# Kernel tuning notes

Measured on AMD Instinct MI355X. Metric: run time of the kernel, lower is better.

## Reference

```python
import jax, jax.numpy as jnp
import numpy as np

B, C, H, W = 4, 256, 64, 64
D = C // 8  # qk projection dim = 32


def setup_inputs() -> dict:
    key = jax.random.key(0)
    ks = jax.random.split(key, 10)
    s = 1.0 / np.sqrt(C)
    return {
        "semantic_map": jax.random.normal(ks[0], (B, C, H, W), jnp.float32),
        "structural_map": jax.random.normal(ks[1], (B, C, H, W), jnp.float32),
        "Wq": jax.random.normal(ks[2], (D, C), jnp.float32) * s,
        "bq": jax.random.normal(ks[3], (D,), jnp.float32) * 0.01,
        "Wk": jax.random.normal(ks[4], (D, C), jnp.float32) * s,
        "bk": jax.random.normal(ks[5], (D,), jnp.float32) * 0.01,
        "Wv": jax.random.normal(ks[6], (C, C), jnp.float32) * s,
        "bv": jax.random.normal(ks[7], (C,), jnp.float32) * 0.01,
        "gamma": jnp.zeros((1,), jnp.float32) + 0.5,  # nonzero so the attention path matters
    }


def reference(semantic_map, structural_map, Wq, bq, Wk, bk, Wv, bv, gamma):
    b, c, h, w = semantic_map.shape
    n = h * w
    # 1x1 convs == per-pixel linear projections
    q = jnp.einsum("bchw,dc->bdhw", semantic_map, Wq) + bq[None, :, None, None]
    k = jnp.einsum("bchw,dc->bdhw", structural_map, Wk) + bk[None, :, None, None]
    v = jnp.einsum("bchw,oc->bohw", structural_map, Wv) + bv[None, :, None, None]
    q = q.reshape(b, -1, n).transpose(0, 2, 1)  # (B, HW, D)
    k = k.reshape(b, -1, n)                     # (B, D, HW)
    v = v.reshape(b, c, n)                      # (B, C, HW)
    energy = jnp.einsum("bid,bdj->bij", q, k)   # (B, HW, HW)
    attention = jax.nn.softmax(energy, axis=-1)
    # out[b,c,i] = sum_j v[b,c,j] * attention[b,i,j]
    out = jnp.einsum("bcj,bij->bci", v, attention).reshape(b, c, h, w)
    return gamma * out + semantic_map
```

## Files before the change

### kernel.cpp

```cpp
#include <hip/hip_runtime.h>

#define B_   4
#define C_   256
#define N_   4096
#define D_   32
#define CP   264

typedef _Float16 half8  __attribute__((ext_vector_type(8)));
typedef _Float16 half4v __attribute__((ext_vector_type(4)));
typedef _Float16 half2v __attribute__((ext_vector_type(2)));
typedef float    f32x4  __attribute__((ext_vector_type(4)));

__global__ __launch_bounds__(256) void wcvt_kernel(
    const float* __restrict__ Wq, const float* __restrict__ Wk,
    const float* __restrict__ Wv, _Float16* __restrict__ Wh)
{
    const int idx = blockIdx.x * 256 + threadIdx.x;
    const int kk  = idx & 31;
    const int row = (idx >> 5) & 15;
    const int kc  = (idx >> 9) & 7;
    const int t   = idx >> 12;
    const int c   = kc*32 + kk;
    float v;
    if (t < 2)      v = Wq[(t*16 + row)*C_ + c];
    else if (t < 4) v = Wk[((t-2)*16 + row)*C_ + c];
    else            v = Wv[((t-4)*16 + row)*C_ + c];
    Wh[idx] = (_Float16)v;
}

__global__ __launch_bounds__(256, 2) void proj_kernel(
    const float* __restrict__ sem, const float* __restrict__ str,
    const _Float16* __restrict__ Wh,
    const float* __restrict__ bq, const float* __restrict__ bk,
    const float* __restrict__ bv,
    _Float16* __restrict__ Qh, _Float16* __restrict__ Kh, _Float16* __restrict__ Vh2)
{
    __shared__ __align__(16) _Float16 s_x[64 * CP];
    __shared__ __align__(16) _Float16 s_s[64 * CP];

    const int bid = blockIdx.x;
    const int h   = bid & 1;
    const int nt6 = (bid >> 1) & 63;
    const int b   = bid >> 7;
    const int n0  = nt6 * 64;
    const int tid = threadIdx.x;
    const int w    = tid >> 6;
    const int lane = tid & 63;
    const int quad = lane >> 4;
    const int l15  = lane & 15;

    const int cnt = (w < 2) ? 3 : 2;
    const int t0  = h*10 + ((w < 2) ? w*3 : 6 + (w-2)*2);
    const bool need_sem = (h == 0);

    f32x4 acc[3][4];
    #pragma unroll
    for (int i = 0; i < 3; ++i)
        #pragma unroll
        for (int j = 0; j < 4; ++j) { acc[i][j][0]=0.f; acc[i][j][1]=0.f; acc[i][j][2]=0.f; acc[i][j][3]=0.f; }

    const size_t xbase = (size_t)b * C_ * N_;

    #pragma unroll
    for (int r = 0; r < 8; ++r) {
        const int slot = r*256 + tid;
        const int nq = slot & 15;
        const int cp = slot >> 4;
        const float* p0 = str + xbase + (size_t)(2*cp) * N_ + n0 + nq*4;
        const float4 a4 = *(const float4*)p0;
        const float4 b4 = *(const float4*)(p0 + N_);
        #pragma unroll
        for (int t = 0; t < 4; ++t) {
            half2v hp; hp[0] = (_Float16)a4[t]; hp[1] = (_Float16)b4[t];
            *(half2v*)(s_x + (nq*4 + t)*CP + 2*cp) = hp;
        }
        if (need_sem) {
            const float* p1 = sem + xbase + (size_t)(2*cp) * N_ + n0 + nq*4;
            const float4 c4 = *(const float4*)p1;
            const float4 d4 = *(const float4*)(p1 + N_);
            #pragma unroll
            for (int t = 0; t < 4; ++t) {
                half2v hp; hp[0] = (_Float16)c4[t]; hp[1] = (_Float16)d4[t];
                *(half2v*)(s_s + (nq*4 + t)*CP + 2*cp) = hp;
            }
        }
    }
    __syncthreads();

    #pragma unroll 1
    for (int kc = 0; kc < 8; ++kc) {
        half8 bfr[4], sfr[4];
        #pragma unroll
        for (int nt = 0; nt < 4; ++nt)
            bfr[nt] = *(const half8*)(s_x + (nt*16 + l15)*CP + kc*32 + quad*8);
        if (w == 0 && need_sem) {
            #pragma unroll
            for (int nt = 0; nt < 4; ++nt)
                sfr[nt] = *(const half8*)(s_s + (nt*16 + l15)*CP + kc*32 + quad*8);
        }
        #pragma unroll
        for (int mi = 0; mi < 3; ++mi) {
            if (mi >= cnt) break;
            const int t = t0 + mi;
            half8 af = *(const half8*)(Wh + ((size_t)((t*8 + kc)*16 + l15))*32 + quad*8);
            #pragma unroll
            for (int nt = 0; nt < 4; ++nt)
                acc[mi][nt] = __builtin_amdgcn_mfma_f32_16x16x32_f16(
                                  af, (t < 2) ? sfr[nt] : bfr[nt], acc[mi][nt], 0, 0, 0);
        }
    }

    #pragma unroll
    for (int mi = 0; mi < 3; ++mi) {
        if (mi >= cnt) break;
        const int t = t0 + mi;
        if (t < 4) {
            const bool isq = (t < 2);
            const int  tt  = isq ? t : (t - 2);
            f32x4 b4 = *(const f32x4*)((isq ? bq : bk) + tt*16 + quad*4);
            _Float16* dst = isq ? Qh : Kh;
            const int dc  = tt*2 + (quad >> 1);
            const int off = (quad & 1) * 4;
            #pragma unroll
            for (int nt = 0; nt < 4; ++nt) {
                const int n = n0 + nt*16 + l15;
                f32x4 a = acc[mi][nt];
                half4v hq;
                hq[0]=(_Float16)(a[0]+b4[0]); hq[1]=(_Float16)(a[1]+b4[1]);
                hq[2]=(_Float16)(a[2]+b4[2]); hq[3]=(_Float16)(a[3]+b4[3]);
                *(half4v*)(dst + ((size_t)(b*4 + dc) * N_ + n) * 8 + off) = hq;
            }
        } else {
            const int ctg = t - 4;
            const int o0  = ctg*16 + quad*4;
            f32x4 b4 = *(const f32x4*)(bv + o0);
            _Float16* vb = Vh2 + (size_t)b * (size_t)N_ * C_;
            #pragma unroll
            for (int nt = 0; nt < 4; ++nt) {
                const int jc  = (n0 >> 4) + nt;
                const int jc2 = jc >> 1;
                const int js  = jc & 1;
                const size_t base = (size_t)jc2 * 8192 + (size_t)ctg * 512 + (size_t)js * 4;
                const int lp = (l15 >> 2) * 16;
                const int e  = l15 & 3;
                f32x4 a = acc[mi][nt];
                #pragma unroll
                for (int r = 0; r < 4; ++r)
                    vb[base + (size_t)(lp + quad*4 + r) * 8 + e] = (_Float16)(a[r] + b4[r]);
            }
        }
    }
}

__global__ __launch_bounds__(256, 2) void flash_kernel(
    const _Float16* __restrict__ Qh, const _Float16* __restrict__ Kh,
    const _Float16* __restrict__ Vh2, const float* __restrict__ sem,
    const float* __restrict__ gma, float* __restrict__ out)
{
    __shared__ float s_mp[4*32];
    __shared__ float s_lp[4*32];
    __shared__ __align__(16) float s_red[4][64][32];

    const int bid = blockIdx.x;
    const int b   = bid >> 7;
    const int i0  = (bid & 127) * 32;
    const int tid = threadIdx.x;
    const int w    = tid >> 6;
    const int lane = tid & 63;
    const int quad = lane >> 4;
    const int l15  = lane & 15;
    const int wc   = w & 1;
    const int wj   = w >> 1;

    const _Float16* qk_base = Qh + (size_t)(b*4 + quad) * N_ * 8;
    const half8 qf0 = *(const half8*)(qk_base + (size_t)(i0 + l15) * 8);
    const half8 qf1 = *(const half8*)(qk_base + (size_t)(i0 + 16 + l15) * 8);

    const _Float16* klane = Kh + ((size_t)(b*4 + quad) * N_ + l15) * 8;
    const _Float16* vl    = Vh2 + (size_t)b * (size_t)N_ * C_
                            + (size_t)(wc*8) * 512 + (size_t)lane * 8;

    float mx0 = -3e38f, mx1 = -3e38f;
    {
        half8 kp[4], kn[4];
        auto kl4 = [&](half8 (&kf)[4], int j0) {
            #pragma unroll
            for (int js = 0; js < 4; ++js)
                kf[js] = *(const half8*)(klane + (size_t)(j0 + js*16) * 8);
        };
        auto p0step = [&](const half8 (&kf)[4], half8 (&kfn)[4], int j0, bool more) {
            if (more) kl4(kfn, j0 + 64);
            #pragma unroll
            for (int js = 0; js < 4; ++js) {
                f32x4 z; z[0]=0.f; z[1]=0.f; z[2]=0.f; z[3]=0.f;
                f32x4 s0 = __builtin_amdgcn_mfma_f32_16x16x32_f16(kf[js], qf0, z, 0, 0, 0);
                f32x4 s1 = __builtin_amdgcn_mfma_f32_16x16x32_f16(kf[js], qf1, z, 0, 0, 0);
                #pragma unroll
                for (int r = 0; r < 4; ++r) { mx0 = fmaxf(mx0, s0[r]); mx1 = fmaxf(mx1, s1[r]); }
            }
        };
        kl4(kp, w*1024);
        #pragma unroll 1
        for (int it2 = 0; it2 < 8; ++it2) {
            const int j0 = w*1024 + it2*128;
            p0step(kp, kn, j0, true);
            p0step(kn, kp, j0 + 64, it2 < 7);
        }
    }
    mx0 = fmaxf(mx0, __shfl_xor(mx0, 16)); mx0 = fmaxf(mx0, __shfl_xor(mx0, 32));
    mx1 = fmaxf(mx1, __shfl_xor(mx1, 16)); mx1 = fmaxf(mx1, __shfl_xor(mx1, 32));
    if (lane < 32) s_mp[w*32 + lane] = (lane < 16) ? mx0 : mx1;
    __syncthreads();
    float mf0 = -3e38f, mf1 = -3e38f;
    #pragma unroll
    for (int ww = 0; ww < 4; ++ww) {
        mf0 = fmaxf(mf0, s_mp[ww*32 + l15]);
        mf1 = fmaxf(mf1, s_mp[ww*32 + 16 + l15]);
    }

    f32x4 acc[8][2];
    #pragma unroll
    for (int ct = 0; ct < 8; ++ct)
        #pragma unroll
        for (int f = 0; f < 2; ++f) { acc[ct][f][0]=0.f; acc[ct][f][1]=0.f; acc[ct][f][2]=0.f; acc[ct][f][3]=0.f; }
    float l0 = 0.f, l1 = 0.f;

    half8 kA[2], kB[2], vA[8], vB[8];

    auto kl2 = [&](half8 (&kf)[2], int j0) {
        kf[0] = *(const half8*)(klane + (size_t)j0 * 8);
        kf[1] = *(const half8*)(klane + (size_t)(j0 + 16) * 8);
    };
    auto vl8 = [&](half8 (&vf)[8], int j0) {
        const _Float16* p = vl + (size_t)(j0 >> 5) * 8192;
        #pragma unroll
        for (int ct = 0; ct < 8; ++ct)
            vf[ct] = *(const half8*)(p + ct*512);
    };

    auto step = [&](const half8 (&kf)[2], const half8 (&vf)[8],
                    half8 (&kfn)[2], half8 (&vfn)[8], int j0, bool more) {
        f32x4 z; z[0]=0.f; z[1]=0.f; z[2]=0.f; z[3]=0.f;
        f32x4 sf0[2], sf1[2];
        #pragma unroll
        for (int js = 0; js < 2; ++js) {
            sf0[js] = __builtin_amdgcn_mfma_f32_16x16x32_f16(kf[js], qf0, z, 0, 0, 0);
            sf1[js] = __builtin_amdgcn_mfma_f32_16x16x32_f16(kf[js], qf1, z, 0, 0, 0);
        }
        if (more) {
            kl2(kfn, j0 + 32);
            vl8(vfn, j0 + 32);
        }
        half4v pf0[2], pf1[2];
        #pragma unroll
        for (int js = 0; js < 2; ++js) {
            float e0 = __expf(sf0[js][0]-mf0), e1 = __expf(sf0[js][1]-mf0);
            float e2 = __expf(sf0[js][2]-mf0), e3 = __expf(sf0[js][3]-mf0);
            l0 += (e0+e1)+(e2+e3);
            half4v p; p[0]=(_Float16)e0; p[1]=(_Float16)e1; p[2]=(_Float16)e2; p[3]=(_Float16)e3;
            pf0[js] = p;
            float f0 = __expf(sf1[js][0]-mf1), f1 = __expf(sf1[js][1]-mf1);
            float f2 = __expf(sf1[js][2]-mf1), f3 = __expf(sf1[js][3]-mf1);
            l1 += (f0+f1)+(f2+f3);
            half4v q; q[0]=(_Float16)f0; q[1]=(_Float16)f1; q[2]=(_Float16)f2; q[3]=(_Float16)f3;
            pf1[js] = q;
        }
        #pragma unroll
        for (int ct = 0; ct < 8; ++ct) {
            half4v vlo = __builtin_shufflevector(vf[ct], vf[ct], 0, 1, 2, 3);
            half4v vhi = __builtin_shufflevector(vf[ct], vf[ct], 4, 5, 6, 7);
            acc[ct][0] = __builtin_amdgcn_mfma_f32_16x16x16f16(vlo, pf0[0], acc[ct][0], 0, 0, 0);
            acc[ct][1] = __builtin_amdgcn_mfma_f32_16x16x16f16(vlo, pf1[0], acc[ct][1], 0, 0, 0);
            acc[ct][0] = __builtin_amdgcn_mfma_f32_16x16x16f16(vhi, pf0[1], acc[ct][0], 0, 0, 0);
            acc[ct][1] = __builtin_amdgcn_mfma_f32_16x16x16f16(vhi, pf1[1], acc[ct][1], 0, 0, 0);
        }
    };

    const int jb = wj * 2048;
    kl2(kA, jb);
    vl8(vA, jb);
    #pragma unroll 1
    for (int s2 = 0; s2 < 32; ++s2) {
        const int j0 = jb + s2*64;
        step(kA, vA, kB, vB, j0, true);
        step(kB, vB, kA, vA, j0 + 32, s2 < 31);
    }

    l0 += __shfl_xor(l0, 16); l0 += __shfl_xor(l0, 32);
    l1 += __shfl_xor(l1, 16); l1 += __shfl_xor(l1, 32);
    if (lane < 32) s_lp[w*32 + lane] = (lane < 16) ? l0 : l1;

    const int kx = (lane & 7) << 2;
    if (wj == 0) {
        #pragma unroll
        for (int t2 = 0; t2 < 4; ++t2) {
            *(f32x4*)&s_red[w][lane][(t2*8)     ^ kx] = acc[4 + t2][0];
            *(f32x4*)&s_red[w][lane][(t2*8 + 4) ^ kx] = acc[4 + t2][1];
        }
    } else {
        #pragma unroll
        for (int t2 = 0; t2 < 4; ++t2) {
            *(f32x4*)&s_red[w][lane][(t2*8)     ^ kx] = acc[t2][0];
            *(f32x4*)&s_red[w][lane][(t2*8 + 4) ^ kx] = acc[t2][1];
        }
    }
    __syncthreads();

    const float lt0 = s_lp[wc*32 + l15]      + s_lp[64 + wc*32 + l15];
    const float lt1 = s_lp[wc*32 + 16 + l15] + s_lp[64 + wc*32 + 16 + l15];
    const float g = gma[0];
    const float sc0 = g / lt0, sc1 = g / lt1;
    const int wp = w ^ 2;

    if (wj == 0) {
        #pragma unroll
        for (int t2 = 0; t2 < 4; ++t2) {
            f32x4 r0 = *(const f32x4*)&s_red[wp][lane][(t2*8)     ^ kx];
            f32x4 r1 = *(const f32x4*)&s_red[wp][lane][(t2*8 + 4) ^ kx];
            r0 += acc[t2][0];
            r1 += acc[t2][1];
            const int cb0 = (wc*8 + t2)*16 + quad*4;
            #pragma unroll
            for (int r4 = 0; r4 < 4; ++r4) {
                const size_t idx = ((size_t)(b*C_ + cb0 + r4)) * N_ + i0 + l15;
                out[idx]      = r0[r4] * sc0 + sem[idx];
                out[idx + 16] = r1[r4] * sc1 + sem[idx + 16];
            }
        }
    } else {
        #pragma unroll
        for (int t2 = 0; t2 < 4; ++t2) {
            f32x4 r0 = *(const f32x4*)&s_red[wp][lane][(t2*8)     ^ kx];
            f32x4 r1 = *(const f32x4*)&s_red[wp][lane][(t2*8 + 4) ^ kx];
            r0 += acc[4 + t2][0];
            r1 += acc[4 + t2][1];
            const int cb0 = (wc*8 + 4 + t2)*16 + quad*4;
            #pragma unroll
            for (int r4 = 0; r4 < 4; ++r4) {
                const size_t idx = ((size_t)(b*C_ + cb0 + r4)) * N_ + i0 + l15;
                out[idx]      = r0[r4] * sc0 + sem[idx];
                out[idx + 16] = r1[r4] * sc1 + sem[idx + 16];
            }
        }
    }
}

extern "C" void kernel_launch(void* const* d_in, const int* in_sizes, int n_in,
                              void* d_out, int out_size, void* d_ws, size_t ws_size,
                              hipStream_t stream) {
    const float* sem = (const float*)d_in[0];
    const float* str = (const float*)d_in[1];
    const float* Wq  = (const float*)d_in[2];
    const float* bq  = (const float*)d_in[3];
    const float* Wk  = (const float*)d_in[4];
    const float* bk  = (const float*)d_in[5];
    const float* Wv  = (const float*)d_in[6];
    const float* bv  = (const float*)d_in[7];
    const float* gma = (const float*)d_in[8];
    float* out = (float*)d_out;

    _Float16* Qh  = (_Float16*)d_ws;
    _Float16* Kh  = Qh + (size_t)B_*N_*D_;
    _Float16* Vh2 = Kh + (size_t)B_*N_*D_;
    _Float16* Wh  = Vh2 + (size_t)B_*C_*N_;

    hipLaunchKernelGGL(wcvt_kernel, dim3(320), dim3(256), 0, stream, Wq, Wk, Wv, Wh);
    hipLaunchKernelGGL(proj_kernel, dim3(B_*(N_/64)*2), dim3(256), 0, stream,
                       sem, str, Wh, bq, bk, bv, Qh, Kh, Vh2);
    hipLaunchKernelGGL(flash_kernel, dim3(B_*(N_/32)), dim3(256), 0, stream,
                       Qh, Kh, Vh2, sem, gma, out);
}
```

Baseline: 169.9 us.

## Merge projection halves into 512-thread blocks, stage V stores, use K=32 MFMA for PV

The projection kernel now runs one 512-thread block per 64-pixel tile instead of two 256-thread halves, so the structural input is loaded and converted once rather than twice. It also double-buffers the weight fragment loads and stages V outputs in shared memory so they can be written with coalesced 16-byte stores. In the flash kernel, P is packed with cvt_pkrtz and the PV product uses 16x16x32 MFMAs in place of pairs of 16x16x16 ones, with s_setprio raised around the MFMA block. The trade-offs are more LDS per projection block (which may lower occupancy) and round-toward-zero conversion of P.

```diff
diff --git a/kernel.cpp b/kernel.cpp
--- a/kernel.cpp
+++ b/kernel.cpp
@@ -28,7 +28,7 @@
     Wh[idx] = (_Float16)v;
 }
 
-__global__ __launch_bounds__(256, 2) void proj_kernel(
+__global__ __launch_bounds__(512, 2) void proj_kernel(
     const float* __restrict__ sem, const float* __restrict__ str,
     const _Float16* __restrict__ Wh,
     const float* __restrict__ bq, const float* __restrict__ bk,
@@ -37,11 +37,11 @@
 {
     __shared__ __align__(16) _Float16 s_x[64 * CP];
     __shared__ __align__(16) _Float16 s_s[64 * CP];
+    __shared__ __align__(16) _Float16 s_v[8][3][1024];
 
     const int bid = blockIdx.x;
-    const int h   = bid & 1;
-    const int nt6 = (bid >> 1) & 63;
-    const int b   = bid >> 7;
+    const int nt6 = bid & 63;
+    const int b   = bid >> 6;
     const int n0  = nt6 * 64;
     const int tid = threadIdx.x;
     const int w    = tid >> 6;
@@ -49,9 +49,8 @@
     const int quad = lane >> 4;
     const int l15  = lane & 15;
 
-    const int cnt = (w < 2) ? 3 : 2;
-    const int t0  = h*10 + ((w < 2) ? w*3 : 6 + (w-2)*2);
-    const bool need_sem = (h == 0);
+    const int cnt = (w < 4) ? 3 : 2;
+    const int t0  = (w < 4) ? w*3 : 12 + (w-4)*2;
 
     f32x4 acc[3][4];
     #pragma unroll
@@ -62,8 +61,8 @@
     const size_t xbase = (size_t)b * C_ * N_;
 
     #pragma unroll
-    for (int r = 0; r < 8; ++r) {
-        const int slot = r*256 + tid;
+    for (int r = 0; r < 4; ++r) {
+        const int slot = r*512 + tid;
         const int nq = slot & 15;
         const int cp = slot >> 4;
         const float* p0 = str + xbase + (size_t)(2*cp) * N_ + n0 + nq*4;
@@ -74,40 +73,58 @@
             half2v hp; hp[0] = (_Float16)a4[t]; hp[1] = (_Float16)b4[t];
             *(half2v*)(s_x + (nq*4 + t)*CP + 2*cp) = hp;
         }
-        if (need_sem) {
-            const float* p1 = sem + xbase + (size_t)(2*cp) * N_ + n0 + nq*4;
-            const float4 c4 = *(const float4*)p1;
-            const float4 d4 = *(const float4*)(p1 + N_);
-            #pragma unroll
-            for (int t = 0; t < 4; ++t) {
-                half2v hp; hp[0] = (_Float16)c4[t]; hp[1] = (_Float16)d4[t];
-                *(half2v*)(s_s + (nq*4 + t)*CP + 2*cp) = hp;
-            }
+        const float* p1 = sem + xbase + (size_t)(2*cp) * N_ + n0 + nq*4;
+        const float4 c4 = *(const float4*)p1;
+        const float4 d4 = *(const float4*)(p1 + N_);
+        #pragma unroll
+        for (int t = 0; t < 4; ++t) {
+            half2v hp; hp[0] = (_Float16)c4[t]; hp[1] = (_Float16)d4[t];
+            *(half2v*)(s_s + (nq*4 + t)*CP + 2*cp) = hp;
         }
     }
     __syncthreads();
 
-    #pragma unroll 1
-    for (int kc = 0; kc < 8; ++kc) {
-        half8 bfr[4], sfr[4];
+    auto afload = [&](half8 (&af)[3], int kc) {
+        #pragma unroll
+        for (int mi = 0; mi < 3; ++mi)
+            if (mi < cnt)
+                af[mi] = *(const half8*)(Wh + ((size_t)(((t0+mi)*8 + kc)*16 + l15))*32 + quad*8);
+    };
+    auto bload = [&](half8 (&bfr)[4], half8 (&sfr)[4], int kc) {
         #pragma unroll
         for (int nt = 0; nt < 4; ++nt)
             bfr[nt] = *(const half8*)(s_x + (nt*16 + l15)*CP + kc*32 + quad*8);
-        if (w == 0 && need_sem) {
+        if (w == 0) {
             #pragma unroll
             for (int nt = 0; nt < 4; ++nt)
                 sfr[nt] = *(const half8*)(s_s + (nt*16 + l15)*CP + kc*32 + quad*8);
         }
+    };
+    auto domfma = [&](const half8 (&af)[3], const half8 (&bfr)[4], const half8 (&sfr)[4]) {
         #pragma unroll
         for (int mi = 0; mi < 3; ++mi) {
             if (mi >= cnt) break;
-            const int t = t0 + mi;
-            half8 af = *(const half8*)(Wh + ((size_t)((t*8 + kc)*16 + l15))*32 + quad*8);
+            const bool useS = (t0 + mi) < 2;
             #pragma unroll
             for (int nt = 0; nt < 4; ++nt)
                 acc[mi][nt] = __builtin_amdgcn_mfma_f32_16x16x32_f16(
-                                  af, (t < 2) ? sfr[nt] : bfr[nt], acc[mi][nt], 0, 0, 0);
-        }
+                                  af[mi], useS ? sfr[nt] : bfr[nt], acc[mi][nt], 0, 0, 0);
+        }
+    };
+
+    half8 afA[3], afB[3];
+    afload(afA, 0);
+    #pragma unroll 1
+    for (int kc2 = 0; kc2 < 4; ++kc2) {
+        const int kc = kc2*2;
+        half8 bfr[4], sfr[4];
+        bload(bfr, sfr, kc);
+        afload(afB, kc+1);
+        domfma(afA, bfr, sfr);
+        half8 bfr2[4], sfr2[4];
+        bload(bfr2, sfr2, kc+1);
+        if (kc2 < 3) afload(afA, kc+2);
+        domfma(afB, bfr2, sfr2);
     }
 
     #pragma unroll
@@ -132,21 +149,33 @@
             }
         } else {
             const int ctg = t - 4;
-            const int o0  = ctg*16 + quad*4;
-            f32x4 b4 = *(const f32x4*)(bv + o0);
-            _Float16* vb = Vh2 + (size_t)b * (size_t)N_ * C_;
+            f32x4 b4 = *(const f32x4*)(bv + ctg*16 + quad*4);
             #pragma unroll
             for (int nt = 0; nt < 4; ++nt) {
-                const int jc  = (n0 >> 4) + nt;
-                const int jc2 = jc >> 1;
-                const int js  = jc & 1;
-                const size_t base = (size_t)jc2 * 8192 + (size_t)ctg * 512 + (size_t)js * 4;
-                const int lp = (l15 >> 2) * 16;
-                const int e  = l15 & 3;
+                const int js = nt & 1;
+                const int hb = nt >> 1;
                 f32x4 a = acc[mi][nt];
                 #pragma unroll
                 for (int r = 0; r < 4; ++r)
-                    vb[base + (size_t)(lp + quad*4 + r) * 8 + e] = (_Float16)(a[r] + b4[r]);
+                    s_v[w][mi][hb*512 + ((l15>>2)*16 + quad*4 + r)*8 + js*4 + (l15&3)]
+                        = (_Float16)(a[r] + b4[r]);
+            }
+        }
+    }
+    {
+        _Float16* vb = Vh2 + (size_t)b * (size_t)N_ * C_;
+        const int jc2_0 = n0 >> 5;
+        #pragma unroll
+        for (int mi = 0; mi < 3; ++mi) {
+            if (mi >= cnt) break;
+            const int t = t0 + mi;
+            if (t >= 4) {
+                const int ctg = t - 4;
+                #pragma unroll
+                for (int hb = 0; hb < 2; ++hb) {
+                    half8 vv = *(const half8*)(&s_v[w][mi][hb*512 + lane*8]);
+                    *(half8*)(vb + (size_t)(jc2_0 + hb)*8192 + (size_t)ctg*512 + lane*8) = vv;
+                }
             }
         }
     }
@@ -237,6 +266,14 @@
         for (int ct = 0; ct < 8; ++ct)
             vf[ct] = *(const half8*)(p + ct*512);
     };
+    auto mkp = [](const f32x4& s, float mf, float& lacc) -> half4v {
+        float e0 = __expf(s[0]-mf), e1 = __expf(s[1]-mf);
+        float e2 = __expf(s[2]-mf), e3 = __expf(s[3]-mf);
+        lacc += (e0+e1)+(e2+e3);
+        half2v p01 = __builtin_bit_cast(half2v, __builtin_amdgcn_cvt_pkrtz(e0, e1));
+        half2v p23 = __builtin_bit_cast(half2v, __builtin_amdgcn_cvt_pkrtz(e2, e3));
+        return __builtin_shufflevector(p01, p23, 0, 1, 2, 3);
+    };
 
     auto step = [&](const half8 (&kf)[2], const half8 (&vf)[8],
                     half8 (&kfn)[2], half8 (&vfn)[8], int j0, bool more) {
@@ -251,29 +288,19 @@
             kl2(kfn, j0 + 32);
             vl8(vfn, j0 + 32);
         }
-        half4v pf0[2], pf1[2];
-        #pragma unroll
-        for (int js = 0; js < 2; ++js) {
-            float e0 = __expf(sf0[js][0]-mf0), e1 = __expf(sf0[js][1]-mf0);
-            float e2 = __expf(sf0[js][2]-mf0), e3 = __expf(sf0[js][3]-mf0);
-            l0 += (e0+e1)+(e2+e3);
-            half4v p; p[0]=(_Float16)e0; p[1]=(_Float16)e1; p[2]=(_Float16)e2; p[3]=(_Float16)e3;
-            pf0[js] = p;
-            float f0 = __expf(sf1[js][0]-mf1), f1 = __expf(sf1[js][1]-mf1);
-            float f2 = __expf(sf1[js][2]-mf1), f3 = __expf(sf1[js][3]-mf1);
-            l1 += (f0+f1)+(f2+f3);
-            half4v q; q[0]=(_Float16)f0; q[1]=(_Float16)f1; q[2]=(_Float16)f2; q[3]=(_Float16)f3;
-            pf1[js] = q;
-        }
+        half4v pa0 = mkp(sf0[0], mf0, l0);
+        half4v pb0 = mkp(sf0[1], mf0, l0);
+        half4v pa1 = mkp(sf1[0], mf1, l1);
+        half4v pb1 = mkp(sf1[1], mf1, l1);
+        half8 pcat0 = __builtin_shufflevector(pa0, pb0, 0, 1, 2, 3, 4, 5, 6, 7);
+        half8 pcat1 = __builtin_shufflevector(pa1, pb1, 0, 1, 2, 3, 4, 5, 6, 7);
+        __builtin_amdgcn_s_setprio(1);
         #pragma unroll
         for (int ct = 0; ct < 8; ++ct) {
-            half4v vlo = __builtin_shufflevector(vf[ct], vf[ct], 0, 1, 2, 3);
-            half4v vhi = __builtin_shufflevector(vf[ct], vf[ct], 4, 5, 6, 7);
-            acc[ct][0] = __builtin_amdgcn_mfma_f32_16x16x16f16(vlo, pf0[0], acc[ct][0], 0, 0, 0);
-            acc[ct][1] = __builtin_amdgcn_mfma_f32_16x16x16f16(vlo, pf1[0], acc[ct][1], 0, 0, 0);
-            acc[ct][0] = __builtin_amdgcn_mfma_f32_16x16x16f16(vhi, pf0[1], acc[ct][0], 0, 0, 0);
-            acc[ct][1] = __builtin_amdgcn_mfma_f32_16x16x16f16(vhi, pf1[1], acc[ct][1], 0, 0, 0);
-        }
+            acc[ct][0] = __builtin_amdgcn_mfma_f32_16x16x32_f16(vf[ct], pcat0, acc[ct][0], 0, 0, 0);
+            acc[ct][1] = __builtin_amdgcn_mfma_f32_16x16x32_f16(vf[ct], pcat1, acc[ct][1], 0, 0, 0);
+        }
+        __builtin_amdgcn_s_setprio(0);
     };
 
     const int jb = wj * 2048;
@@ -365,7 +392,7 @@
     _Float16* Wh  = Vh2 + (size_t)B_*C_*N_;
 
     hipLaunchKernelGGL(wcvt_kernel, dim3(320), dim3(256), 0, stream, Wq, Wk, Wv, Wh);
-    hipLaunchKernelGGL(proj_kernel, dim3(B_*(N_/64)*2), dim3(256), 0, stream,
+    hipLaunchKernelGGL(proj_kernel, dim3(B_*(N_/64)), dim3(512), 0, stream,
                        sem, str, Wh, bq, bk, bv, Qh, Kh, Vh2);
     hipLaunchKernelGGL(flash_kernel, dim3(B_*(N_/32)), dim3(256), 0, stream,
                        Qh, Kh, Vh2, sem, gma, out);
```

Result: faster. 157.1 us (-7.6%).
